# Kernel optimization log

Hardware: AMD Instinct MI355X
Metric: run time of the kernel (lower is better)

The kernel has to match this reference:

```python
import jax, jax.numpy as jnp
import numpy as np
from jax import lax

WIN = 9
EPS = 1e-05
PAD = WIN // 2


def _box_sum_axis(x, axis):
    # 1D ones-kernel conv (zero padded) along one spatial axis of [N,C,D,H,W].
    kshape = [1, 1, 1, 1, 1]
    kshape[axis] = WIN
    kernel = jnp.ones(kshape, dtype=x.dtype)
    pad = [(0, 0), (0, 0), (0, 0)]
    pad[axis - 2] = (PAD, PAD)
    return lax.conv_general_dilated(
        x, kernel, window_strides=(1, 1, 1), padding=pad,
        dimension_numbers=('NCDHW', 'OIDHW', 'NCDHW'))


def box_sum(x):
    # Separable box filter == dense 9x9x9 ones conv with zero padding.
    for ax in (2, 3, 4):
        x = _box_sum_axis(x, ax)
    return x


def setup_inputs() -> dict:
    key = jax.random.key(0)
    k1, k2 = jax.random.split(key)
    shape = (1, 1, 192, 224, 192)
    I = jax.random.uniform(k1, shape, dtype=jnp.float32)
    J = jax.random.uniform(k2, shape, dtype=jnp.float32)
    return {"I": I, "J": J}


def reference(I, J):
    win_size = float(WIN ** 3)
    I_sum = box_sum(I)
    J_sum = box_sum(J)
    I2_sum = box_sum(I * I)
    J2_sum = box_sum(J * J)
    IJ_sum = box_sum(I * J)

    u_I = I_sum / win_size
    u_J = J_sum / win_size
    cross = IJ_sum - u_J * I_sum - u_I * J_sum + u_I * u_J * win_size
    I_var = I2_sum - 2.0 * u_I * I_sum + u_I * u_I * win_size
    J_var = J2_sum - 2.0 * u_J * J_sum + u_J * u_J * win_size
    cc = cross * cross / (I_var * J_var + EPS)
    return -1.0 * jnp.mean(cc)
```

## Files before the change

### kernel.cpp

```cpp
#include <hip/hip_runtime.h>

#define DD 192
#define HH 224
#define WW 192
#define HWN (HH*WW)
#define PLANE ((size_t)DD*HWN)
#define DSEG 32
#define HS 28
#define NHS 8
#define NPART (DD*NHS)

__global__ __launch_bounds__(192) void kA(
    const float* __restrict__ I, const float* __restrict__ J,
    float* __restrict__ F, int chunk_base, int chunk)
{
    const int h  = blockIdx.x;
    const int d0 = chunk_base + blockIdx.y * DSEG;
    const int wv = threadIdx.x >> 6;
    const int l  = threadIdx.x & 63;
    const int w0 = wv << 6;

    __shared__ float stg[3][2][2][72];
    float (*st)[2][72] = stg[wv];

#pragma unroll
    for (int b = 0; b < 2; ++b) {
        st[b][0][l] = 0.f; st[b][1][l] = 0.f;
        if (l < 8) { st[b][0][64 + l] = 0.f; st[b][1][64 + l] = 0.f; }
    }

    const size_t fs   = (size_t)chunk * HWN;
    const size_t rowb = (size_t)h * WW;
    const int  cm = w0 - 4 + l;
    const int  ch = w0 + 60 + l;
    const bool vm = (cm >= 0) && (cm < WW);
    const bool vh = (l < 8) && (ch < WW);

    float r0[9], r1[9], r2[9], r3[9], r4[9];
    float S0=0.f,S1=0.f,S2=0.f,S3=0.f,S4=0.f;
#pragma unroll
    for (int k = 0; k < 9; ++k) { r0[k]=0.f; r1[k]=0.f; r2[k]=0.f; r3[k]=0.f; r4[k]=0.f; }

    for (int bse = 0; bse < 54; bse += 18) {
#pragma unroll
        for (int k = 0; k < 18; ++k) {
            int s = bse + k;
            if (s < DSEG + 8) {
                const int slot = (k < 9) ? k : k - 9;
                const int buf  = k & 1;
                int din = d0 - 4 + s;
                float a0, a1, a2, a3, a4;
                if (din >= 0 && din < DD) {
                    const float* Ip = I + (size_t)din * HWN + rowb;
                    const float* Jp = J + (size_t)din * HWN + rowb;
                    if (vm) {
                        st[buf][0][l] = Ip[cm];
                        st[buf][1][l] = Jp[cm];
                    }
                    if (vh) {
                        st[buf][0][64 + l] = Ip[ch];
                        st[buf][1][64 + l] = Jp[ch];
                    }
                    a0=a1=a2=a3=a4=0.f;
#pragma unroll
                    for (int j = 0; j < 9; ++j) {
                        float vi = st[buf][0][l + j];
                        float vj = st[buf][1][l + j];
                        a0 += vi;
                        a1 += vj;
                        a2 = fmaf(vi, vi, a2);
                        a3 = fmaf(vj, vj, a3);
                        a4 = fmaf(vi, vj, a4);
                    }
                } else {
                    a0=a1=a2=a3=a4=0.f;
                }
                S0 += a0 - r0[slot]; r0[slot] = a0;
                S1 += a1 - r1[slot]; r1[slot] = a1;
                S2 += a2 - r2[slot]; r2[slot] = a2;
                S3 += a3 - r3[slot]; r3[slot] = a3;
                S4 += a4 - r4[slot]; r4[slot] = a4;

                int dc = din - 4;
                if (dc >= d0 && dc < d0 + DSEG) {
                    size_t o = (size_t)(dc - chunk_base) * HWN + rowb
                             + (size_t)(w0 + l);
                    F[o]        = S0;
                    F[fs + o]   = S1;
                    F[2*fs + o] = S2;
                    F[3*fs + o] = S3;
                    F[4*fs + o] = S4;
                }
            }
        }
    }
}

__global__ __launch_bounds__(192) void kB(
    const float* __restrict__ F, double* __restrict__ partials,
    int chunk_base, int chunk)
{
    const int drel = blockIdx.x;
    const int hs   = blockIdx.y;
    const int w    = threadIdx.x;
    const int h0   = hs * HS;
    const size_t fs = (size_t)chunk * HWN;
    const float* __restrict__ B = F + (size_t)drel * HWN + (size_t)w;

    float r0[9], r1[9], r2[9], r3[9], r4[9];
    float S0=0.f,S1=0.f,S2=0.f,S3=0.f,S4=0.f;
#pragma unroll
    for (int k = 0; k < 9; ++k) { r0[k]=0.f; r1[k]=0.f; r2[k]=0.f; r3[k]=0.f; r4[k]=0.f; }

    float acc = 0.f;

    float c0=0.f,c1=0.f,c2=0.f,c3=0.f,c4=0.f;
    {
        int hin = h0 - 4;
        if (hin >= 0) {
            size_t o = (size_t)hin * WW;
            c0=B[o]; c1=B[fs+o]; c2=B[2*fs+o]; c3=B[3*fs+o]; c4=B[4*fs+o];
        }
    }

    for (int bse = 0; bse < 36; bse += 9) {
#pragma unroll
        for (int k = 0; k < 9; ++k) {
            int s = bse + k;

            float n0=0.f,n1=0.f,n2=0.f,n3=0.f,n4=0.f;
            int hin1 = h0 - 3 + s;
            if (s < 35 && hin1 >= 0 && hin1 < HH) {
                size_t o = (size_t)hin1 * WW;
                n0=B[o]; n1=B[fs+o]; n2=B[2*fs+o]; n3=B[3*fs+o]; n4=B[4*fs+o];
            }

            S0 += c0 - r0[k]; r0[k] = c0;
            S1 += c1 - r1[k]; r1[k] = c1;
            S2 += c2 - r2[k]; r2[k] = c2;
            S3 += c3 - r3[k]; r3[k] = c3;
            S4 += c4 - r4[k]; r4[k] = c4;

            if (s >= 8) {
                const float inv = 1.0f / 729.0f;
                float cross = S4 - S0 * S1 * inv;
                float varI  = S2 - S0 * S0 * inv;
                float varJ  = S3 - S1 * S1 * inv;
                acc += cross * cross / (varI * varJ + 1e-5f);
            }

            c0=n0; c1=n1; c2=n2; c3=n3; c4=n4;
        }
    }

    __shared__ float red[192];
    red[w] = acc;
    __syncthreads();
#pragma unroll
    for (int off = 96; off >= 3; off >>= 1) {
        if (w < off) red[w] += red[w + off];
        __syncthreads();
    }
    if (w == 0) {
        int d = chunk_base + drel;
        partials[d * NHS + hs] = (double)(red[0] + red[1] + red[2]);
    }
}

__global__ __launch_bounds__(256) void k3_reduce(
    const double* __restrict__ partials, float* __restrict__ out)
{
    __shared__ double red[256];
    int t = threadIdx.x;
    double a = 0.0;
    for (int i = t; i < NPART; i += 256) a += partials[i];
    red[t] = a;
    __syncthreads();
    for (int off = 128; off > 0; off >>= 1) {
        if (t < off) red[t] += red[t + off];
        __syncthreads();
    }
    if (t == 0) out[0] = (float)(-red[0] / (double)PLANE);
}

extern "C" void kernel_launch(void* const* d_in, const int* in_sizes, int n_in,
                              void* d_out, int out_size, void* d_ws, size_t ws_size,
                              hipStream_t stream)
{
    const float* I = (const float*)d_in[0];
    const float* J = (const float*)d_in[1];
    float* out = (float*)d_out;

    double* partials = (double*)d_ws;
    const size_t part_bytes = 16384;
    float* F = (float*)((char*)d_ws + part_bytes);

    static const int chunks[4] = {192, 96, 64, 32};
    int chunk = 32;
    for (int i = 0; i < 4; ++i) {
        size_t need = part_bytes + 5ull * (size_t)chunks[i] * HWN * sizeof(float);
        if (need <= ws_size) { chunk = chunks[i]; break; }
    }

    for (int cb = 0; cb < DD; cb += chunk) {
        kA<<<dim3(HH, chunk / DSEG), dim3(192), 0, stream>>>(I, J, F, cb, chunk);
        kB<<<dim3(chunk, NHS), dim3(192), 0, stream>>>(F, partials, cb, chunk);
    }
    k3_reduce<<<dim3(1), dim3(256), 0, stream>>>(partials, out);
}
```

Measured before the change: 78.58 us.

## Interleave box-sum intermediates as float4 plus scalar, prefetch next depth slice

Stores four of the five W/D-filtered sums interleaved as float4 (plus a separate scalar array) so kB does one vector load and one scalar load per row instead of five strided loads. kA now software-prefetches the next depth slice into registers while computing the current one, writing it into the alternate shared buffer afterwards. DSEG is halved to 16, which doubles kA's grid and adds more halo recomputation along depth. The 16-slice halo step count changes, raising the ratio of redundant loads per output slice.

```diff
diff --git a/kernel.cpp b/kernel.cpp
--- a/kernel.cpp
+++ b/kernel.cpp
@@ -5,14 +5,16 @@
 #define WW 192
 #define HWN (HH*WW)
 #define PLANE ((size_t)DD*HWN)
-#define DSEG 32
+#define DSEG 16
+#define NSTEP (DSEG + 8)
 #define HS 28
 #define NHS 8
 #define NPART (DD*NHS)
 
 __global__ __launch_bounds__(192) void kA(
     const float* __restrict__ I, const float* __restrict__ J,
-    float* __restrict__ F, int chunk_base, int chunk)
+    float4* __restrict__ F4, float* __restrict__ F1,
+    int chunk_base, int chunk)
 {
     const int h  = blockIdx.x;
     const int d0 = chunk_base + blockIdx.y * DSEG;
@@ -29,7 +31,6 @@
         if (l < 8) { st[b][0][64 + l] = 0.f; st[b][1][64 + l] = 0.f; }
     }
 
-    const size_t fs   = (size_t)chunk * HWN;
     const size_t rowb = (size_t)h * WW;
     const int  cm = w0 - 4 + l;
     const int  ch = w0 + 60 + l;
@@ -41,71 +42,79 @@
 #pragma unroll
     for (int k = 0; k < 9; ++k) { r0[k]=0.f; r1[k]=0.f; r2[k]=0.f; r3[k]=0.f; r4[k]=0.f; }
 
-    for (int bse = 0; bse < 54; bse += 18) {
+    {
+        int din = d0 - 4;
+        bool pv = (din >= 0) && (din < DD);
+        float pI=0.f, pJ=0.f, qI=0.f, qJ=0.f;
+        const float* Ip = I + (size_t)din * HWN + rowb;
+        const float* Jp = J + (size_t)din * HWN + rowb;
+        if (pv && vm) { pI = Ip[cm]; pJ = Jp[cm]; }
+        if (pv && vh) { qI = Ip[ch]; qJ = Jp[ch]; }
+        if (vm) { st[0][0][l] = pI;      st[0][1][l] = pJ; }
+        if (vh) { st[0][0][64 + l] = qI; st[0][1][64 + l] = qJ; }
+    }
+
+    for (int bse = 0; bse < 36; bse += 18) {
 #pragma unroll
         for (int k = 0; k < 18; ++k) {
             int s = bse + k;
-            if (s < DSEG + 8) {
-                const int slot = (k < 9) ? k : k - 9;
+            if (s < NSTEP) {
+                const int slot = k % 9;
                 const int buf  = k & 1;
-                int din = d0 - 4 + s;
-                float a0, a1, a2, a3, a4;
-                if (din >= 0 && din < DD) {
+
+                float nI=0.f, nJ=0.f, mI=0.f, mJ=0.f;
+                {
+                    int din = d0 - 3 + s;
+                    bool pv = (s + 1 < NSTEP) && (din >= 0) && (din < DD);
                     const float* Ip = I + (size_t)din * HWN + rowb;
                     const float* Jp = J + (size_t)din * HWN + rowb;
-                    if (vm) {
-                        st[buf][0][l] = Ip[cm];
-                        st[buf][1][l] = Jp[cm];
-                    }
-                    if (vh) {
-                        st[buf][0][64 + l] = Ip[ch];
-                        st[buf][1][64 + l] = Jp[ch];
-                    }
-                    a0=a1=a2=a3=a4=0.f;
-#pragma unroll
-                    for (int j = 0; j < 9; ++j) {
-                        float vi = st[buf][0][l + j];
-                        float vj = st[buf][1][l + j];
-                        a0 += vi;
-                        a1 += vj;
-                        a2 = fmaf(vi, vi, a2);
-                        a3 = fmaf(vj, vj, a3);
-                        a4 = fmaf(vi, vj, a4);
-                    }
-                } else {
-                    a0=a1=a2=a3=a4=0.f;
+                    if (pv && vm) { nI = Ip[cm]; nJ = Jp[cm]; }
+                    if (pv && vh) { mI = Ip[ch]; mJ = Jp[ch]; }
                 }
+
+                float a0=0.f,a1=0.f,a2=0.f,a3=0.f,a4=0.f;
+#pragma unroll
+                for (int j = 0; j < 9; ++j) {
+                    float vi = st[buf][0][l + j];
+                    float vj = st[buf][1][l + j];
+                    a0 += vi;
+                    a1 += vj;
+                    a2 = fmaf(vi, vi, a2);
+                    a3 = fmaf(vj, vj, a3);
+                    a4 = fmaf(vi, vj, a4);
+                }
+
                 S0 += a0 - r0[slot]; r0[slot] = a0;
                 S1 += a1 - r1[slot]; r1[slot] = a1;
                 S2 += a2 - r2[slot]; r2[slot] = a2;
                 S3 += a3 - r3[slot]; r3[slot] = a3;
                 S4 += a4 - r4[slot]; r4[slot] = a4;
 
-                int dc = din - 4;
-                if (dc >= d0 && dc < d0 + DSEG) {
+                int dc = d0 - 8 + s;
+                if (s >= 8) {
                     size_t o = (size_t)(dc - chunk_base) * HWN + rowb
                              + (size_t)(w0 + l);
-                    F[o]        = S0;
-                    F[fs + o]   = S1;
-                    F[2*fs + o] = S2;
-                    F[3*fs + o] = S3;
-                    F[4*fs + o] = S4;
+                    F4[o] = make_float4(S0, S1, S2, S3);
+                    F1[o] = S4;
                 }
+
+                if (vm) { st[buf^1][0][l] = nI;      st[buf^1][1][l] = nJ; }
+                if (vh) { st[buf^1][0][64 + l] = mI; st[buf^1][1][64 + l] = mJ; }
             }
         }
     }
 }
 
 __global__ __launch_bounds__(192) void kB(
-    const float* __restrict__ F, double* __restrict__ partials,
-    int chunk_base, int chunk)
+    const float4* __restrict__ F4, const float* __restrict__ F1,
+    double* __restrict__ partials, int chunk_base, int chunk)
 {
     const int drel = blockIdx.x;
     const int hs   = blockIdx.y;
     const int w    = threadIdx.x;
     const int h0   = hs * HS;
-    const size_t fs = (size_t)chunk * HWN;
-    const float* __restrict__ B = F + (size_t)drel * HWN + (size_t)w;
+    const float4* __restrict__ B4 = F4 + (size_t)drel * HWN + (size_t)w;
+    const float*  __restrict__ B1 = F1 + (size_t)drel * HWN + (size_t)w;
 
     float r0[9], r1[9], r2[9], r3[9], r4[9];
     float S0=0.f,S1=0.f,S2=0.f,S3=0.f,S4=0.f;
@@ -119,7 +128,8 @@
         int hin = h0 - 4;
         if (hin >= 0) {
             size_t o = (size_t)hin * WW;
-            c0=B[o]; c1=B[fs+o]; c2=B[2*fs+o]; c3=B[3*fs+o]; c4=B[4*fs+o];
+            float4 v = B4[o];
+            c0=v.x; c1=v.y; c2=v.z; c3=v.w; c4=B1[o];
         }
     }
 
@@ -132,7 +142,8 @@
             int hin1 = h0 - 3 + s;
             if (s < 35 && hin1 >= 0 && hin1 < HH) {
                 size_t o = (size_t)hin1 * WW;
-                n0=B[o]; n1=B[fs+o]; n2=B[2*fs+o]; n3=B[3*fs+o]; n4=B[4*fs+o];
+                float4 v = B4[o];
+                n0=v.x; n1=v.y; n2=v.z; n3=v.w; n4=B1[o];
             }
 
             S0 += c0 - r0[k]; r0[k] = c0;
@@ -193,18 +204,20 @@
 
     double* partials = (double*)d_ws;
     const size_t part_bytes = 16384;
-    float* F = (float*)((char*)d_ws + part_bytes);
-
-    static const int chunks[4] = {192, 96, 64, 32};
-    int chunk = 32;
-    for (int i = 0; i < 4; ++i) {
-        size_t need = part_bytes + 5ull * (size_t)chunks[i] * HWN * sizeof(float);
+
+    static const int chunks[6] = {192, 96, 64, 48, 32, 16};
+    int chunk = 16;
+    for (int i = 0; i < 6; ++i) {
+        size_t need = part_bytes + 20ull * (size_t)chunks[i] * HWN;
         if (need <= ws_size) { chunk = chunks[i]; break; }
     }
 
+    float4* F4 = (float4*)((char*)d_ws + part_bytes);
+    float*  F1 = (float*)((char*)d_ws + part_bytes + 16ull * (size_t)chunk * HWN);
+
     for (int cb = 0; cb < DD; cb += chunk) {
-        kA<<<dim3(HH, chunk / DSEG), dim3(192), 0, stream>>>(I, J, F, cb, chunk);
-        kB<<<dim3(chunk, NHS), dim3(192), 0, stream>>>(F, partials, cb, chunk);
+        kA<<<dim3(HH, chunk / DSEG), dim3(192), 0, stream>>>(I, J, F4, F1, cb, chunk);
+        kB<<<dim3(chunk, NHS), dim3(192), 0, stream>>>(F4, F1, partials, cb, chunk);
     }
     k3_reduce<<<dim3(1), dim3(256), 0, stream>>>(partials, out);
 }
```

Result: slower. 82.17 us (+4.6%).
